# Kernel optimization log

Hardware: AMD Instinct MI355X
Metric: run time of the kernel (lower is better)

The kernel has to match this reference:

```python
import jax, jax.numpy as jnp
import numpy as np

# 27 kernel taps x 3 offset components (dz, dy, dx), matching the module's offset0 list.
OFFSET0 = np.array([
    1, 1, 1, 1, 1, 0, 1, 1, -1, 1, 0, 1, 1, 0, 0, 1, 0, -1, 1, -1, 1, 1, -1, 0, 1, -1, -1,
    0, 1, 1, 0, 1, 0, 0, 1, -1, 0, 0, 1, 0, 0, 0, 0, 0, -1, 0, -1, 1, 0, -1, 0, 0, -1, -1,
    -1, 1, 1, -1, 1, 0, -1, 1, -1, -1, 0, 1, -1, 0, 0, -1, 0, -1, -1, -1, 1, -1, -1, 0, -1, -1, -1
], dtype=np.float64).reshape(27, 3)

BN_EPS = 1e-5


def upsample_nearest2(x):
    # nn.Upsample(scale_factor=2), default mode='nearest', on [B,C,Z,Y,X]
    x = jnp.repeat(x, 2, axis=2)
    x = jnp.repeat(x, 2, axis=3)
    return jnp.repeat(x, 2, axis=4)


def deform_conv3d_static(x, W, b, alpha):
    """3D deformable conv, kernel 3, pad 1, stride 1, with spatially-constant
    per-tap offsets alpha*OFFSET0. Zero padding outside; trilinear sampling.
    Since offsets are static, each tap samples at a fixed fractional shift,
    implemented as a static trilinear combination of slices of the padded input.
    x: [B,C,Z,Y,X], W: [O,C,3,3,3], b: [O].
    """
    B, C, Z, Y, X = x.shape
    # pad 2: 1 for the 3x3x3 kernel + 1 for fractional offsets (|alpha*d| <= 0.7)
    xp = jnp.pad(x, ((0, 0), (0, 0), (2, 2), (2, 2), (2, 2)))
    out = None
    t = 0
    for kz in range(3):
        for ky in range(3):
            for kx in range(3):
                dz, dy, dx = (alpha * OFFSET0[t]).tolist()
                s = (kz - 1 + dz, ky - 1 + dy, kx - 1 + dx)  # shift rel. to output voxel
                f = [int(np.floor(v)) for v in s]
                w = [v - fl for v, fl in zip(s, f)]
                vol = None
                for cz in (0, 1):
                    for cy in (0, 1):
                        for cx in (0, 1):
                            wt = ((w[0] if cz else 1.0 - w[0]) *
                                  (w[1] if cy else 1.0 - w[1]) *
                                  (w[2] if cx else 1.0 - w[2]))
                            if wt == 0.0:
                                continue
                            z0 = 2 + f[0] + cz
                            y0 = 2 + f[1] + cy
                            x0 = 2 + f[2] + cx
                            sl = xp[:, :, z0:z0 + Z, y0:y0 + Y, x0:x0 + X]
                            sl = jnp.float32(wt) * sl
                            vol = sl if vol is None else vol + sl
                contrib = jnp.einsum('oc,bczyx->bozyx', W[:, :, kz, ky, kx], vol)
                out = contrib if out is None else out + contrib
                t += 1
    return out + b[None, :, None, None, None]


def batchnorm(x, g, bt, m, v):
    # eval-mode BatchNorm3d over channel axis 1
    inv = g * jax.lax.rsqrt(v + BN_EPS)
    return x * inv[None, :, None, None, None] + (bt - m * inv)[None, :, None, None, None]


def setup_inputs() -> dict:
    key = jax.random.key(0)
    ks = jax.random.split(key, 13)
    ch_in, ch_out = 64, 32
    x = jax.random.normal(ks[0], (1, ch_in, 32, 32, 32), jnp.float32)
    w_def = jax.random.normal(ks[1], (ch_out, ch_in, 3, 3, 3), jnp.float32) * 0.05
    b_def = jax.random.normal(ks[2], (ch_out,), jnp.float32) * 0.05
    bn1_g = 1.0 + 0.1 * jax.random.normal(ks[3], (ch_out,), jnp.float32)
    bn1_b = 0.1 * jax.random.normal(ks[4], (ch_out,), jnp.float32)
    bn1_m = 0.1 * jax.random.normal(ks[5], (ch_out,), jnp.float32)
    bn1_v = jax.random.uniform(ks[6], (ch_out,), jnp.float32, 0.5, 1.5)
    w_comb = jax.random.normal(ks[7], (ch_out, 3 * ch_out), jnp.float32) * 0.1
    b_comb = 0.05 * jax.random.normal(ks[8], (ch_out,), jnp.float32)
    bn2_g = 1.0 + 0.1 * jax.random.normal(ks[9], (ch_out,), jnp.float32)
    bn2_b = 0.1 * jax.random.normal(ks[10], (ch_out,), jnp.float32)
    bn2_m = 0.1 * jax.random.normal(ks[11], (ch_out,), jnp.float32)
    bn2_v = jax.random.uniform(ks[12], (ch_out,), jnp.float32, 0.5, 1.5)
    return {"x": x, "w_def": w_def, "b_def": b_def,
            "bn1_g": bn1_g, "bn1_b": bn1_b, "bn1_m": bn1_m, "bn1_v": bn1_v,
            "w_comb": w_comb, "b_comb": b_comb,
            "bn2_g": bn2_g, "bn2_b": bn2_b, "bn2_m": bn2_m, "bn2_v": bn2_v}


def reference(x, w_def, b_def, bn1_g, bn1_b, bn1_m, bn1_v,
              w_comb, b_comb, bn2_g, bn2_b, bn2_m, bn2_v):
    xu = upsample_nearest2(x)
    branches = []
    for alpha in (0.0, 0.4, 0.7):  # shared deform-conv weights, three static offset scales
        o = deform_conv3d_static(xu, w_def, b_def, alpha)
        o = jax.nn.relu(batchnorm(o, bn1_g, bn1_b, bn1_m, bn1_v))
        branches.append(o)
    cat = jnp.concatenate(branches, axis=1)  # [B, 3*ch_out, Z,Y,X]
    y = jnp.einsum('oc,bczyx->bozyx', w_comb, cat) + b_comb[None, :, None, None, None]
    y = batchnorm(y, bn2_g, bn2_b, bn2_m, bn2_v)
    return jax.nn.relu(y)
```

## Files before the change

kernel.cpp:

```cpp
#include <hip/hip_runtime.h>


typedef __bf16 bf16x8 __attribute__((ext_vector_type(8)));
typedef float f32x16 __attribute__((ext_vector_type(16)));
typedef unsigned u32x2 __attribute__((ext_vector_type(2)));

__device__ inline unsigned short f2bf(float f) {
  unsigned int u = __float_as_uint(f);
  u += 0x7FFFu + ((u >> 16) & 1u);
  return (unsigned short)(u >> 16);
}

__device__ inline bf16x8 bc16(uint4 v) { return __builtin_bit_cast(bf16x8, v); }

__device__ inline unsigned cvtpk(float lo, float hi) {
  unsigned r;
  asm("v_cvt_pk_bf16_f32 %0, %1, %2" : "=v"(r) : "v"(lo), "v"(hi));
  return r;
}

__device__ inline void plswap(unsigned& a, unsigned& b) {
  u32x2 r = __builtin_amdgcn_permlane32_swap(a, b, false, false);
  a = r.x;
  b = r.y;
}

__device__ inline void gload16(const unsigned short* g, unsigned short* l) {
  __builtin_amdgcn_global_load_lds(
      (const __attribute__((address_space(1))) unsigned int*)(const void*)g,
      (__attribute__((address_space(3))) unsigned int*)(void*)l, 16, 0, 0);
}

__device__ inline float ucoef(int abit, int k, int jbit, float alpha) {
  if (abit == 0) return (k == 0) ? (jbit ? alpha : 1.f - alpha) : (jbit ? 1.f : 0.f);
  return (k == 2) ? (jbit ? 1.f - alpha : alpha) : (jbit ? 0.f : 1.f);
}

__global__ void k_prep(const float* __restrict__ x, unsigned short* __restrict__ xT,
                       const float* __restrict__ w_def, const float* __restrict__ bn1_g,
                       const float* __restrict__ bn1_v, unsigned short* __restrict__ W_sw,
                       const float* __restrict__ w_comb, const float* __restrict__ b_comb,
                       const float* __restrict__ bn2_g, const float* __restrict__ bn2_b,
                       const float* __restrict__ bn2_m, const float* __restrict__ bn2_v,
                       const float* __restrict__ b_def, const float* __restrict__ bn1_b,
                       const float* __restrict__ bn1_m, unsigned short* __restrict__ W2_sw,
                       float* __restrict__ bias1, float* __restrict__ bias2) {
  __shared__ unsigned short t[64][65];
  int bid = blockIdx.x;
  if (bid < 512) {
    int s0 = bid * 64;
    int lane = threadIdx.x & 63;
    int grp = threadIdx.x >> 6;
#pragma unroll
    for (int c = grp; c < 64; c += 4)
      t[c][lane] = f2bf(x[c * 32768 + s0 + lane]);
    __syncthreads();
#pragma unroll
    for (int s = grp; s < 64; s += 4)
      xT[(size_t)(s0 + s) * 64 + lane] = t[lane][s];
  } else if (bid < 2048) {
    int e = (bid - 512) * 256 + threadIdx.x;
    int j = e & 7;
    int lane = (e >> 3) & 63;
    int idx = e >> 9;
    int nt = idx % 3;
    idx /= 3;
    int s = idx & 31;
    int p = idx >> 5;
    int o = lane & 31;
    int br = nt;
    int kk = 16 * s + ((lane >> 5) << 3) + j;
    int tap = kk >> 6, ch = kk & 63;
    int jz = (tap >> 2) & 1, jy = (tap >> 1) & 1, jx = tap & 1;
    int a = (p >> 2) & 1, b = (p >> 1) & 1, cp = p & 1;
    float alpha = (br == 0) ? 0.f : ((br == 1) ? 0.4f : 0.7f);
    const float* wb = w_def + (o * 64 + ch) * 27;
    float sum = 0.f;
    for (int kz = 0; kz < 3; ++kz) {
      float uz = ucoef(a, kz, jz, alpha);
      if (uz == 0.f) continue;
      for (int ky = 0; ky < 3; ++ky) {
        float uy = ucoef(b, ky, jy, alpha);
        if (uy == 0.f) continue;
        float uzy = uz * uy;
        for (int kx = 0; kx < 3; ++kx) {
          float ux = ucoef(cp, kx, jx, alpha);
          if (ux != 0.f) sum += wb[kz * 9 + ky * 3 + kx] * uzy * ux;
        }
      }
    }
    float s1 = bn1_g[o] * rsqrtf(bn1_v[o] + 1e-5f);
    W_sw[e] = f2bf(sum * s1);
  } else {
    int tid = threadIdx.x;
    for (int e = tid; e < 3072; e += 256) {
      int j = e & 7;
      int lane = (e >> 3) & 63;
      int s2 = e >> 9;
      int n = lane & 31;
      int k = 16 * s2 + ((lane >> 5) << 3) + j;
      float sc2 = bn2_g[n] * rsqrtf(bn2_v[n] + 1e-5f);
      W2_sw[e] = f2bf(w_comb[n * 96 + k] * sc2);
    }
    if (tid < 32) {
      float s1 = bn1_g[tid] * rsqrtf(bn1_v[tid] + 1e-5f);
      bias1[tid] = (b_def[tid] - bn1_m[tid]) * s1 + bn1_b[tid];
      float s2 = bn2_g[tid] * rsqrtf(bn2_v[tid] + 1e-5f);
      bias2[tid] = (b_comb[tid] - bn2_m[tid]) * s2 + bn2_b[tid];
    }
  }
}

__launch_bounds__(512, 2)
__global__ void k_main(const unsigned short* __restrict__ xT,
                       const unsigned short* __restrict__ W_sw,
                       const unsigned short* __restrict__ W2_sw,
                       const float* __restrict__ bias1f,
                       const float* __restrict__ bias2f,
                       float* __restrict__ out) {
  __shared__ unsigned short xt[51840];
  __shared__ unsigned short wring[2][12288];
  __shared__ float blds[64];
  int tid = threadIdx.x;
  int lane = tid & 63;
  int wv = tid >> 6;
  int bid = blockIdx.x;
  int bph = bid & 1, a = (bid >> 1) & 1;
  int tb = bid >> 2;
  int tx = tb & 3, ty = (tb >> 2) & 3, tz = tb >> 4;
  int i0 = tz * 8, j0 = ty * 8, k0 = tx * 8;

  for (int t2 = tid; t2 < 6480; t2 += 512) {
    int cblk = t2 & 7;
    int r = t2 >> 3;
    int xrel = r % 10;
    int zy = r / 10;
    int yrel = zy % 9;
    int zrel = zy / 9;
    int gz = i0 + a - 1 + zrel, gy = j0 + bph - 1 + yrel, gx = k0 - 1 + xrel;
    uint4 v = make_uint4(0u, 0u, 0u, 0u);
    if ((unsigned)gz < 32u && (unsigned)gy < 32u && (unsigned)gx < 32u)
      v = *(const uint4*)(xT + ((((gz * 32 + gy) * 32 + gx) << 6) + (cblk << 3)));
    *(uint4*)(xt + ((r << 6) + (((cblk + r) << 3) & 63))) = v;
  }
  if (tid < 32) {
    blds[tid] = bias1f[tid];
    blds[32 + tid] = bias2f[tid];
  }

  bf16x8 b2f[6];
  const uint4* w2q = (const uint4*)W2_sw;
#pragma unroll
  for (int s2 = 0; s2 < 6; ++s2) b2f[s2] = bc16(w2q[s2 * 64 + lane]);
  __syncthreads();

  int h = lane >> 5, h8 = h << 3;
  int m = lane & 31;
  int ax = m & 7, ay = (m >> 3) & 1, az = m >> 4;
  int zs = wv >> 2, ys = wv & 3;
  int dz0 = 4 * zs + az;
  int dy = 2 * ys + ay;
  int p0 = (a << 2) | (bph << 1);

  auto stage = [&](int cc) {
    int pn = p0 | (cc >> 2);
    const unsigned short* g =
        W_sw + (size_t)pn * 49152 + (cc & 3) * 12288 + wv * 1536 + lane * 8;
    unsigned short* l = &wring[cc & 1][wv * 1536];
    gload16(g, l);
    gload16(g + 512, l + 512);
    gload16(g + 1024, l + 1024);
  };

  stage(0);

  f32x16 osv0, osv1;
  f32x16 acc[2][3];
#pragma unroll
  for (int mt = 0; mt < 2; ++mt)
#pragma unroll
    for (int nt = 0; nt < 3; ++nt) acc[mt][nt] = (f32x16)0.f;

  int qr = (wv & 3) * 2;

  for (int cc = 0; cc < 8; ++cc) {
    asm volatile("s_waitcnt vmcnt(0)" ::: "memory");
    __builtin_amdgcn_s_barrier();
    __builtin_amdgcn_sched_barrier(0);
    if (cc < 7) stage(cc + 1);
    __builtin_amdgcn_sched_barrier(0);
    int cp = cc >> 2;
    int tb2 = (cc & 3) * 2;
    const unsigned short* wfb = &wring[cc & 1][lane * 8];
#pragma unroll
    for (int i = 0; i < 8; ++i) {
      int q2 = (i + qr) & 7;
      int tl = q2 >> 2, q = q2 & 3;
      int t8 = tb2 + tl;
      int jz = (t8 >> 2) & 1, jy = (t8 >> 1) & 1, jx = t8 & 1;
      int row0 = ((dz0 + jz) * 9 + (dy + jy)) * 10 + (ax + cp + jx);
      int row1 = row0 + 180;
      int c0 = (q << 4) + h8;
      int e0 = (row0 << 6) + ((c0 + (row0 << 3)) & 63);
      int e1 = (row1 << 6) + ((c0 + (row1 << 3)) & 63);
      bf16x8 a0 = bc16(*(const uint4*)(xt + e0));
      bf16x8 a1 = bc16(*(const uint4*)(xt + e1));
      const unsigned short* wf = wfb + tl * 6144 + q * 1536;
      bf16x8 bb0 = bc16(*(const uint4*)(wf));
      bf16x8 bb1 = bc16(*(const uint4*)(wf + 512));
      bf16x8 bb2 = bc16(*(const uint4*)(wf + 1024));
      __builtin_amdgcn_s_setprio(1);
      acc[0][0] = __builtin_amdgcn_mfma_f32_32x32x16_bf16(bb0, a0, acc[0][0], 0, 0, 0);
      acc[1][0] = __builtin_amdgcn_mfma_f32_32x32x16_bf16(bb0, a1, acc[1][0], 0, 0, 0);
      acc[0][1] = __builtin_amdgcn_mfma_f32_32x32x16_bf16(bb1, a0, acc[0][1], 0, 0, 0);
      acc[1][1] = __builtin_amdgcn_mfma_f32_32x32x16_bf16(bb1, a1, acc[1][1], 0, 0, 0);
      acc[0][2] = __builtin_amdgcn_mfma_f32_32x32x16_bf16(bb2, a0, acc[0][2], 0, 0, 0);
      acc[1][2] = __builtin_amdgcn_mfma_f32_32x32x16_bf16(bb2, a1, acc[1][2], 0, 0, 0);
      __builtin_amdgcn_s_setprio(0);
    }

    if (cc == 3) {
#pragma unroll
      for (int mt = 0; mt < 2; ++mt) {
        uint4 fr[6];
#pragma unroll
        for (int nt = 0; nt < 3; ++nt) {
          unsigned ww[8];
#pragma unroll
          for (int qc = 0; qc < 8; ++qc) {
            int q = qc >> 1, c2 = qc & 1;
            int r0 = 4 * q + 2 * c2;
            int row = (r0 & 3) + ((r0 >> 2) << 3) + (h << 2);
            float lo = fmaxf(acc[mt][nt][r0] + blds[row], 0.f);
            float hi = fmaxf(acc[mt][nt][r0 + 1] + blds[row + 1], 0.f);
            ww[2 * q + c2] = cvtpk(lo, hi);
          }
          plswap(ww[0], ww[2]);
          plswap(ww[1], ww[3]);
          plswap(ww[4], ww[6]);
          plswap(ww[5], ww[7]);
          fr[2 * nt] = make_uint4(ww[0], ww[1], ww[2], ww[3]);
          fr[2 * nt + 1] = make_uint4(ww[4], ww[5], ww[6], ww[7]);
        }
        f32x16 acc2 = (f32x16)0.f;
#pragma unroll
        for (int s2 = 0; s2 < 6; ++s2)
          acc2 = __builtin_amdgcn_mfma_f32_32x32x16_bf16(b2f[s2], bc16(fr[s2]), acc2, 0, 0, 0);
        f32x16 ov;
#pragma unroll
        for (int r = 0; r < 16; ++r) {
          int row = (r & 3) + ((r >> 2) << 3) + (h << 2);
          ov[r] = fmaxf(acc2[r] + blds[32 + row], 0.f);
        }
        if (mt == 0) osv0 = ov; else osv1 = ov;
#pragma unroll
        for (int nt = 0; nt < 3; ++nt) acc[mt][nt] = (f32x16)0.f;
      }
    }
  }

#pragma unroll
  for (int mt = 0; mt < 2; ++mt) {
    uint4 fr[6];
#pragma unroll
    for (int nt = 0; nt < 3; ++nt) {
      unsigned ww[8];
#pragma unroll
      for (int qc = 0; qc < 8; ++qc) {
        int q = qc >> 1, c2 = qc & 1;
        int r0 = 4 * q + 2 * c2;
        int row = (r0 & 3) + ((r0 >> 2) << 3) + (h << 2);
        float lo = fmaxf(acc[mt][nt][r0] + blds[row], 0.f);
        float hi = fmaxf(acc[mt][nt][r0 + 1] + blds[row + 1], 0.f);
        ww[2 * q + c2] = cvtpk(lo, hi);
      }
      plswap(ww[0], ww[2]);
      plswap(ww[1], ww[3]);
      plswap(ww[4], ww[6]);
      plswap(ww[5], ww[7]);
      fr[2 * nt] = make_uint4(ww[0], ww[1], ww[2], ww[3]);
      fr[2 * nt + 1] = make_uint4(ww[4], ww[5], ww[6], ww[7]);
    }
    f32x16 acc2 = (f32x16)0.f;
#pragma unroll
    for (int s2 = 0; s2 < 6; ++s2)
      acc2 = __builtin_amdgcn_mfma_f32_32x32x16_bf16(b2f[s2], bc16(fr[s2]), acc2, 0, 0, 0);
    f32x16 prev = (mt == 0) ? osv0 : osv1;
    int Z = 2 * (i0 + 4 * zs + 2 * mt + az) + a;
    int Y = 2 * (j0 + dy) + bph;
    float2* o2 = (float2*)out;
#pragma unroll
    for (int r = 0; r < 16; ++r) {
      int ch = (r & 3) + ((r >> 2) << 3) + (h << 2);
      float v1 = fmaxf(acc2[r] + blds[32 + ch], 0.f);
      o2[((size_t)ch << 17) + ((size_t)Z << 11) + (Y << 5) + (k0 + ax)] =
          make_float2(prev[r], v1);
    }
  }
}

extern "C" void kernel_launch(void* const* d_in, const int* in_sizes, int n_in,
                              void* d_out, int out_size, void* d_ws, size_t ws_size,
                              hipStream_t stream) {
  (void)in_sizes; (void)n_in; (void)out_size; (void)ws_size;
  const float* x      = (const float*)d_in[0];
  const float* w_def  = (const float*)d_in[1];
  const float* b_def  = (const float*)d_in[2];
  const float* bn1_g  = (const float*)d_in[3];
  const float* bn1_b  = (const float*)d_in[4];
  const float* bn1_m  = (const float*)d_in[5];
  const float* bn1_v  = (const float*)d_in[6];
  const float* w_comb = (const float*)d_in[7];
  const float* b_comb = (const float*)d_in[8];
  const float* bn2_g  = (const float*)d_in[9];
  const float* bn2_b  = (const float*)d_in[10];
  const float* bn2_m  = (const float*)d_in[11];
  const float* bn2_v  = (const float*)d_in[12];

  char* ws = (char*)d_ws;
  unsigned short* xT   = (unsigned short*)(ws);
  unsigned short* W_sw = (unsigned short*)(ws + 4194304);
  unsigned short* W2sw = (unsigned short*)(ws + 4980736);
  float* bias1 = (float*)(ws + 4986880);
  float* bias2 = (float*)(ws + 4987008);
  float* out = (float*)d_out;

  hipLaunchKernelGGL(k_prep, dim3(2049), dim3(256), 0, stream,
                     x, xT, w_def, bn1_g, bn1_v, W_sw,
                     w_comb, b_comb, bn2_g, bn2_b, bn2_m, bn2_v,
                     b_def, bn1_b, bn1_m, W2sw, bias1, bias2);
  hipLaunchKernelGGL(k_main, dim3(256), dim3(512), 0, stream,
                     xT, W_sw, W2sw, bias1, bias2, out);
}
```

Measured before the change: 52.91 us.

## Read input activations directly from global memory instead of an LDS halo tile

The LDS staging of the input halo tile is removed. The main kernel now loads MFMA A-fragments straight from a channel-quartered bf16 layout in global memory, with a zeroed pad region standing in for out-of-bounds voxels. Blocks shrink to 256 threads and the grid doubles to 512, with a reordered block-to-tile mapping. The second-stage weights are reloaded from global memory on demand rather than held in registers. This frees LDS and registers for occupancy and drops the staging loop, at the cost of more global and L2 traffic with less reuse of the halo across taps.

Result: no change. 53.74 us (+1.6%).

```diff
diff --git a/kernel.cpp b/kernel.cpp
--- a/kernel.cpp
+++ b/kernel.cpp
@@ -36,7 +36,10 @@
   return (k == 2) ? (jbit ? 1.f - alpha : alpha) : (jbit ? 0.f : 1.f);
 }
 
-__global__ void k_prep(const float* __restrict__ x, unsigned short* __restrict__ xT,
+#define XREG_USH 524352
+#define XZERO_B 1048576u
+
+__global__ void k_prep(const float* __restrict__ x, unsigned short* __restrict__ xT2,
                        const float* __restrict__ w_def, const float* __restrict__ bn1_g,
                        const float* __restrict__ bn1_v, unsigned short* __restrict__ W_sw,
                        const float* __restrict__ w_comb, const float* __restrict__ b_comb,
@@ -55,9 +58,10 @@
     for (int c = grp; c < 64; c += 4)
       t[c][lane] = f2bf(x[c * 32768 + s0 + lane]);
     __syncthreads();
+    int q = lane >> 4, e = lane & 15;
 #pragma unroll
     for (int s = grp; s < 64; s += 4)
-      xT[(size_t)(s0 + s) * 64 + lane] = t[lane][s];
+      xT2[q * XREG_USH + (size_t)(s0 + s) * 16 + e] = t[lane][s];
   } else if (bid < 2048) {
     int e = (bid - 512) * 256 + threadIdx.x;
     int j = e & 7;
@@ -102,6 +106,10 @@
       float sc2 = bn2_g[n] * rsqrtf(bn2_v[n] + 1e-5f);
       W2_sw[e] = f2bf(w_comb[n * 96 + k] * sc2);
     }
+    {
+      int q = tid >> 6, e2 = tid & 63;
+      xT2[q * XREG_USH + 524288 + e2] = 0;
+    }
     if (tid < 32) {
       float s1 = bn1_g[tid] * rsqrtf(bn1_v[tid] + 1e-5f);
       bias1[tid] = (b_def[tid] - bn1_m[tid]) * s1 + bn1_b[tid];
@@ -111,67 +119,51 @@
   }
 }
 
-__launch_bounds__(512, 2)
-__global__ void k_main(const unsigned short* __restrict__ xT,
+__launch_bounds__(256, 2)
+__global__ void k_main(const unsigned short* __restrict__ xT2,
                        const unsigned short* __restrict__ W_sw,
                        const unsigned short* __restrict__ W2_sw,
                        const float* __restrict__ bias1f,
                        const float* __restrict__ bias2f,
                        float* __restrict__ out) {
-  __shared__ unsigned short xt[51840];
   __shared__ unsigned short wring[2][12288];
   __shared__ float blds[64];
   int tid = threadIdx.x;
   int lane = tid & 63;
   int wv = tid >> 6;
   int bid = blockIdx.x;
-  int bph = bid & 1, a = (bid >> 1) & 1;
-  int tb = bid >> 2;
+  int tb = (bid & 7) | ((bid >> 5) << 3);
+  int ph = (bid >> 3) & 3;
+  int bph = ph & 1, a = ph >> 1;
   int tx = tb & 3, ty = (tb >> 2) & 3, tz = tb >> 4;
-  int i0 = tz * 8, j0 = ty * 8, k0 = tx * 8;
-
-  for (int t2 = tid; t2 < 6480; t2 += 512) {
-    int cblk = t2 & 7;
-    int r = t2 >> 3;
-    int xrel = r % 10;
-    int zy = r / 10;
-    int yrel = zy % 9;
-    int zrel = zy / 9;
-    int gz = i0 + a - 1 + zrel, gy = j0 + bph - 1 + yrel, gx = k0 - 1 + xrel;
-    uint4 v = make_uint4(0u, 0u, 0u, 0u);
-    if ((unsigned)gz < 32u && (unsigned)gy < 32u && (unsigned)gx < 32u)
-      v = *(const uint4*)(xT + ((((gz * 32 + gy) * 32 + gx) << 6) + (cblk << 3)));
-    *(uint4*)(xt + ((r << 6) + (((cblk + r) << 3) & 63))) = v;
-  }
+  int i0 = tz * 4, j0 = ty * 8, k0 = tx * 8;
+
   if (tid < 32) {
     blds[tid] = bias1f[tid];
     blds[32 + tid] = bias2f[tid];
   }
 
-  bf16x8 b2f[6];
-  const uint4* w2q = (const uint4*)W2_sw;
-#pragma unroll
-  for (int s2 = 0; s2 < 6; ++s2) b2f[s2] = bc16(w2q[s2 * 64 + lane]);
-  __syncthreads();
-
-  int h = lane >> 5, h8 = h << 3;
+  int h = lane >> 5;
   int m = lane & 31;
   int ax = m & 7, ay = (m >> 3) & 1, az = m >> 4;
-  int zs = wv >> 2, ys = wv & 3;
-  int dz0 = 4 * zs + az;
-  int dy = 2 * ys + ay;
   int p0 = (a << 2) | (bph << 1);
+  unsigned hb = (unsigned)(h << 4);
+
+  const char* xq0 = (const char*)xT2;
+  const char* xq1 = xq0 + 1048704;
+  const char* xq2 = xq0 + 2097408;
+  const char* xq3 = xq0 + 3146112;
 
   auto stage = [&](int cc) {
     int pn = p0 | (cc >> 2);
     const unsigned short* g =
-        W_sw + (size_t)pn * 49152 + (cc & 3) * 12288 + wv * 1536 + lane * 8;
-    unsigned short* l = &wring[cc & 1][wv * 1536];
-    gload16(g, l);
-    gload16(g + 512, l + 512);
-    gload16(g + 1024, l + 1024);
+        W_sw + pn * 49152 + (cc & 3) * 12288 + wv * 3072 + lane * 8;
+    unsigned short* l = &wring[cc & 1][wv * 3072];
+#pragma unroll
+    for (int k = 0; k < 6; ++k) gload16(g + k * 512, l + k * 512);
   };
 
+  __syncthreads();
   stage(0);
 
   f32x16 osv0, osv1;
@@ -180,8 +172,6 @@
   for (int mt = 0; mt < 2; ++mt)
 #pragma unroll
     for (int nt = 0; nt < 3; ++nt) acc[mt][nt] = (f32x16)0.f;
-
-  int qr = (wv & 3) * 2;
 
   for (int cc = 0; cc < 8; ++cc) {
     asm volatile("s_waitcnt vmcnt(0)" ::: "memory");
@@ -189,37 +179,52 @@
     __builtin_amdgcn_sched_barrier(0);
     if (cc < 7) stage(cc + 1);
     __builtin_amdgcn_sched_barrier(0);
-    int cp = cc >> 2;
-    int tb2 = (cc & 3) * 2;
+
+    int cp = cc >> 2, jy = cc & 1, jz = (cc >> 1) & 1;
+    int gz0i = i0 + a - 1 + az + jz;
+    int gz1i = gz0i + 2;
+    int gyi = j0 + bph - 1 + 2 * wv + ay + jy;
+    int gx0i = k0 - 1 + ax + cp;
+    int gx1i = gx0i + 1;
+    bool oky = (unsigned)gyi < 32u;
+    bool okz0 = (unsigned)gz0i < 32u, okz1 = (unsigned)gz1i < 32u;
+    bool okx0 = (unsigned)gx0i < 32u, okx1 = (unsigned)gx1i < 32u;
+    unsigned s00 = (unsigned)(((gz0i * 32 + gyi) * 32 + gx0i) * 32) + hb;
+    unsigned s01 = (unsigned)(((gz1i * 32 + gyi) * 32 + gx0i) * 32) + hb;
+    unsigned s10 = (unsigned)(((gz0i * 32 + gyi) * 32 + gx1i) * 32) + hb;
+    unsigned s11 = (unsigned)(((gz1i * 32 + gyi) * 32 + gx1i) * 32) + hb;
+    unsigned v00 = (oky && okz0 && okx0) ? s00 : XZERO_B;
+    unsigned v01 = (oky && okz1 && okx0) ? s01 : XZERO_B;
+    unsigned v10 = (oky && okz0 && okx1) ? s10 : XZERO_B;
+    unsigned v11 = (oky && okz1 && okx1) ? s11 : XZERO_B;
+
     const unsigned short* wfb = &wring[cc & 1][lane * 8];
 #pragma unroll
-    for (int i = 0; i < 8; ++i) {
-      int q2 = (i + qr) & 7;
-      int tl = q2 >> 2, q = q2 & 3;
-      int t8 = tb2 + tl;
-      int jz = (t8 >> 2) & 1, jy = (t8 >> 1) & 1, jx = t8 & 1;
-      int row0 = ((dz0 + jz) * 9 + (dy + jy)) * 10 + (ax + cp + jx);
-      int row1 = row0 + 180;
-      int c0 = (q << 4) + h8;
-      int e0 = (row0 << 6) + ((c0 + (row0 << 3)) & 63);
-      int e1 = (row1 << 6) + ((c0 + (row1 << 3)) & 63);
-      bf16x8 a0 = bc16(*(const uint4*)(xt + e0));
-      bf16x8 a1 = bc16(*(const uint4*)(xt + e1));
-      const unsigned short* wf = wfb + tl * 6144 + q * 1536;
-      bf16x8 bb0 = bc16(*(const uint4*)(wf));
-      bf16x8 bb1 = bc16(*(const uint4*)(wf + 512));
-      bf16x8 bb2 = bc16(*(const uint4*)(wf + 1024));
-      __builtin_amdgcn_s_setprio(1);
-      acc[0][0] = __builtin_amdgcn_mfma_f32_32x32x16_bf16(bb0, a0, acc[0][0], 0, 0, 0);
-      acc[1][0] = __builtin_amdgcn_mfma_f32_32x32x16_bf16(bb0, a1, acc[1][0], 0, 0, 0);
-      acc[0][1] = __builtin_amdgcn_mfma_f32_32x32x16_bf16(bb1, a0, acc[0][1], 0, 0, 0);
-      acc[1][1] = __builtin_amdgcn_mfma_f32_32x32x16_bf16(bb1, a1, acc[1][1], 0, 0, 0);
-      acc[0][2] = __builtin_amdgcn_mfma_f32_32x32x16_bf16(bb2, a0, acc[0][2], 0, 0, 0);
-      acc[1][2] = __builtin_amdgcn_mfma_f32_32x32x16_bf16(bb2, a1, acc[1][2], 0, 0, 0);
-      __builtin_amdgcn_s_setprio(0);
+    for (int tl = 0; tl < 2; ++tl) {
+      unsigned va0 = tl ? v10 : v00;
+      unsigned va1 = tl ? v11 : v01;
+#pragma unroll
+      for (int q = 0; q < 4; ++q) {
+        const char* xb = (q == 0) ? xq0 : (q == 1) ? xq1 : (q == 2) ? xq2 : xq3;
+        bf16x8 a0 = bc16(*(const uint4*)(xb + va0));
+        bf16x8 a1 = bc16(*(const uint4*)(xb + va1));
+        const unsigned short* wf = wfb + tl * 6144 + q * 1536;
+        bf16x8 bb0 = bc16(*(const uint4*)(wf));
+        bf16x8 bb1 = bc16(*(const uint4*)(wf + 512));
+        bf16x8 bb2 = bc16(*(const uint4*)(wf + 1024));
+        __builtin_amdgcn_s_setprio(1);
+        acc[0][0] = __builtin_amdgcn_mfma_f32_32x32x16_bf16(bb0, a0, acc[0][0], 0, 0, 0);
+        acc[1][0] = __builtin_amdgcn_mfma_f32_32x32x16_bf16(bb0, a1, acc[1][0], 0, 0, 0);
+        acc[0][1] = __builtin_amdgcn_mfma_f32_32x32x16_bf16(bb1, a0, acc[0][1], 0, 0, 0);
+        acc[1][1] = __builtin_amdgcn_mfma_f32_32x32x16_bf16(bb1, a1, acc[1][1], 0, 0, 0);
+        acc[0][2] = __builtin_amdgcn_mfma_f32_32x32x16_bf16(bb2, a0, acc[0][2], 0, 0, 0);
+        acc[1][2] = __builtin_amdgcn_mfma_f32_32x32x16_bf16(bb2, a1, acc[1][2], 0, 0, 0);
+        __builtin_amdgcn_s_setprio(0);
+      }
     }
 
     if (cc == 3) {
+      const uint4* w2q = (const uint4*)W2_sw;
 #pragma unroll
       for (int mt = 0; mt < 2; ++mt) {
         uint4 fr[6];
@@ -245,7 +250,8 @@
         f32x16 acc2 = (f32x16)0.f;
 #pragma unroll
         for (int s2 = 0; s2 < 6; ++s2)
-          acc2 = __builtin_amdgcn_mfma_f32_32x32x16_bf16(b2f[s2], bc16(fr[s2]), acc2, 0, 0, 0);
+          acc2 = __builtin_amdgcn_mfma_f32_32x32x16_bf16(bc16(w2q[s2 * 64 + lane]),
+                                                         bc16(fr[s2]), acc2, 0, 0, 0);
         f32x16 ov;
 #pragma unroll
         for (int r = 0; r < 16; ++r) {
@@ -259,42 +265,46 @@
     }
   }
 
-#pragma unroll
-  for (int mt = 0; mt < 2; ++mt) {
-    uint4 fr[6];
-#pragma unroll
-    for (int nt = 0; nt < 3; ++nt) {
-      unsigned ww[8];
-#pragma unroll
-      for (int qc = 0; qc < 8; ++qc) {
-        int q = qc >> 1, c2 = qc & 1;
-        int r0 = 4 * q + 2 * c2;
-        int row = (r0 & 3) + ((r0 >> 2) << 3) + (h << 2);
-        float lo = fmaxf(acc[mt][nt][r0] + blds[row], 0.f);
-        float hi = fmaxf(acc[mt][nt][r0 + 1] + blds[row + 1], 0.f);
-        ww[2 * q + c2] = cvtpk(lo, hi);
-      }
-      plswap(ww[0], ww[2]);
-      plswap(ww[1], ww[3]);
-      plswap(ww[4], ww[6]);
-      plswap(ww[5], ww[7]);
-      fr[2 * nt] = make_uint4(ww[0], ww[1], ww[2], ww[3]);
-      fr[2 * nt + 1] = make_uint4(ww[4], ww[5], ww[6], ww[7]);
-    }
-    f32x16 acc2 = (f32x16)0.f;
-#pragma unroll
-    for (int s2 = 0; s2 < 6; ++s2)
-      acc2 = __builtin_amdgcn_mfma_f32_32x32x16_bf16(b2f[s2], bc16(fr[s2]), acc2, 0, 0, 0);
-    f32x16 prev = (mt == 0) ? osv0 : osv1;
-    int Z = 2 * (i0 + 4 * zs + 2 * mt + az) + a;
-    int Y = 2 * (j0 + dy) + bph;
-    float2* o2 = (float2*)out;
-#pragma unroll
-    for (int r = 0; r < 16; ++r) {
-      int ch = (r & 3) + ((r >> 2) << 3) + (h << 2);
-      float v1 = fmaxf(acc2[r] + blds[32 + ch], 0.f);
-      o2[((size_t)ch << 17) + ((size_t)Z << 11) + (Y << 5) + (k0 + ax)] =
-          make_float2(prev[r], v1);
+  {
+    const uint4* w2q = (const uint4*)W2_sw;
+#pragma unroll
+    for (int mt = 0; mt < 2; ++mt) {
+      uint4 fr[6];
+#pragma unroll
+      for (int nt = 0; nt < 3; ++nt) {
+        unsigned ww[8];
+#pragma unroll
+        for (int qc = 0; qc < 8; ++qc) {
+          int q = qc >> 1, c2 = qc & 1;
+          int r0 = 4 * q + 2 * c2;
+          int row = (r0 & 3) + ((r0 >> 2) << 3) + (h << 2);
+          float lo = fmaxf(acc[mt][nt][r0] + blds[row], 0.f);
+          float hi = fmaxf(acc[mt][nt][r0 + 1] + blds[row + 1], 0.f);
+          ww[2 * q + c2] = cvtpk(lo, hi);
+        }
+        plswap(ww[0], ww[2]);
+        plswap(ww[1], ww[3]);
+        plswap(ww[4], ww[6]);
+        plswap(ww[5], ww[7]);
+        fr[2 * nt] = make_uint4(ww[0], ww[1], ww[2], ww[3]);
+        fr[2 * nt + 1] = make_uint4(ww[4], ww[5], ww[6], ww[7]);
+      }
+      f32x16 acc2 = (f32x16)0.f;
+#pragma unroll
+      for (int s2 = 0; s2 < 6; ++s2)
+        acc2 = __builtin_amdgcn_mfma_f32_32x32x16_bf16(bc16(w2q[s2 * 64 + lane]),
+                                                       bc16(fr[s2]), acc2, 0, 0, 0);
+      f32x16 prev = (mt == 0) ? osv0 : osv1;
+      int Z = 2 * (i0 + 2 * mt + az) + a;
+      int Y = 2 * (j0 + 2 * wv + ay) + bph;
+      float2* o2 = (float2*)out;
+#pragma unroll
+      for (int r = 0; r < 16; ++r) {
+        int ch = (r & 3) + ((r >> 2) << 3) + (h << 2);
+        float v1 = fmaxf(acc2[r] + blds[32 + ch], 0.f);
+        o2[((size_t)ch << 17) + ((size_t)Z << 11) + (Y << 5) + (k0 + ax)] =
+            make_float2(prev[r], v1);
+      }
     }
   }
 }
@@ -318,17 +328,17 @@
   const float* bn2_v  = (const float*)d_in[12];
 
   char* ws = (char*)d_ws;
-  unsigned short* xT   = (unsigned short*)(ws);
-  unsigned short* W_sw = (unsigned short*)(ws + 4194304);
-  unsigned short* W2sw = (unsigned short*)(ws + 4980736);
-  float* bias1 = (float*)(ws + 4986880);
-  float* bias2 = (float*)(ws + 4987008);
+  unsigned short* xT2  = (unsigned short*)(ws);
+  unsigned short* W_sw = (unsigned short*)(ws + 4194816);
+  unsigned short* W2sw = (unsigned short*)(ws + 4981248);
+  float* bias1 = (float*)(ws + 4987392);
+  float* bias2 = (float*)(ws + 4987520);
   float* out = (float*)d_out;
 
   hipLaunchKernelGGL(k_prep, dim3(2049), dim3(256), 0, stream,
-                     x, xT, w_def, bn1_g, bn1_v, W_sw,
+                     x, xT2, w_def, bn1_g, bn1_v, W_sw,
                      w_comb, b_comb, bn2_g, bn2_b, bn2_m, bn2_v,
                      b_def, bn1_b, bn1_m, W2sw, bias1, bias2);
-  hipLaunchKernelGGL(k_main, dim3(256), dim3(512), 0, stream,
-                     xT, W_sw, W2sw, bias1, bias2, out);
-}
+  hipLaunchKernelGGL(k_main, dim3(512), dim3(256), 0, stream,
+                     xT2, W_sw, W2sw, bias1, bias2, out);
+}
```

## Use triple-buffered weight ring with finer chunks and prefetch depth two

Applied to the files above, without the earlier changes.

Replaces the double-buffered weight staging (8 chunks of two taps each) with a triple-buffered ring of 16 single-tap chunks, prefetching two chunks ahead and waiting with vmcnt(2) instead of draining all loads each iteration. Only six of the eight waves issue the global-to-LDS loads. The per-wave rotation of the tap/quarter order (qr) is dropped. The aim is to hide weight-load latency behind MFMA work, at the cost of twice as many barriers and less compute between them, plus possible LDS bank conflicts now that all waves read in the same order.

Measured after the change: 52.72 us, median of 2. About the same (-0.4%).

```diff
diff --git a/kernel.cpp b/kernel.cpp
--- a/kernel.cpp
+++ b/kernel.cpp
@@ -119,7 +119,7 @@
                        const float* __restrict__ bias2f,
                        float* __restrict__ out) {
   __shared__ unsigned short xt[51840];
-  __shared__ unsigned short wring[2][12288];
+  __shared__ unsigned short wring[3][6144];
   __shared__ float blds[64];
   int tid = threadIdx.x;
   int lane = tid & 63;
@@ -162,17 +162,19 @@
   int dy = 2 * ys + ay;
   int p0 = (a << 2) | (bph << 1);
 
-  auto stage = [&](int cc) {
-    int pn = p0 | (cc >> 2);
-    const unsigned short* g =
-        W_sw + (size_t)pn * 49152 + (cc & 3) * 12288 + wv * 1536 + lane * 8;
-    unsigned short* l = &wring[cc & 1][wv * 1536];
-    gload16(g, l);
-    gload16(g + 512, l + 512);
-    gload16(g + 1024, l + 1024);
+  auto stage = [&](int c, int slot) {
+    if (wv < 6) {
+      int pn = p0 | (c >> 3);
+      const unsigned short* g =
+          W_sw + (size_t)pn * 49152 + (c & 7) * 6144 + wv * 1024 + lane * 8;
+      unsigned short* l = &wring[slot][wv * 1024];
+      gload16(g, l);
+      gload16(g + 512, l + 512);
+    }
   };
 
-  stage(0);
+  stage(0, 0);
+  stage(1, 1);
 
   f32x16 osv0, osv1;
   f32x16 acc[2][3];
@@ -181,31 +183,30 @@
 #pragma unroll
     for (int nt = 0; nt < 3; ++nt) acc[mt][nt] = (f32x16)0.f;
 
-  int qr = (wv & 3) * 2;
-
-  for (int cc = 0; cc < 8; ++cc) {
-    asm volatile("s_waitcnt vmcnt(0)" ::: "memory");
+  for (int c = 0; c < 16; ++c) {
+    if (c < 15) {
+      asm volatile("s_waitcnt vmcnt(2)" ::: "memory");
+    } else {
+      asm volatile("s_waitcnt vmcnt(0)" ::: "memory");
+    }
     __builtin_amdgcn_s_barrier();
     __builtin_amdgcn_sched_barrier(0);
-    if (cc < 7) stage(cc + 1);
+    if (c < 14) stage(c + 2, (c + 2) % 3);
     __builtin_amdgcn_sched_barrier(0);
-    int cp = cc >> 2;
-    int tb2 = (cc & 3) * 2;
-    const unsigned short* wfb = &wring[cc & 1][lane * 8];
-#pragma unroll
-    for (int i = 0; i < 8; ++i) {
-      int q2 = (i + qr) & 7;
-      int tl = q2 >> 2, q = q2 & 3;
-      int t8 = tb2 + tl;
-      int jz = (t8 >> 2) & 1, jy = (t8 >> 1) & 1, jx = t8 & 1;
-      int row0 = ((dz0 + jz) * 9 + (dy + jy)) * 10 + (ax + cp + jx);
-      int row1 = row0 + 180;
+
+    int cp = c >> 3, t8 = c & 7;
+    int jz = (t8 >> 2) & 1, jy = (t8 >> 1) & 1, jx = t8 & 1;
+    int row0 = ((dz0 + jz) * 9 + (dy + jy)) * 10 + (ax + cp + jx);
+    int row1 = row0 + 180;
+    const unsigned short* wfb = &wring[c % 3][lane * 8];
+#pragma unroll
+    for (int q = 0; q < 4; ++q) {
       int c0 = (q << 4) + h8;
       int e0 = (row0 << 6) + ((c0 + (row0 << 3)) & 63);
       int e1 = (row1 << 6) + ((c0 + (row1 << 3)) & 63);
       bf16x8 a0 = bc16(*(const uint4*)(xt + e0));
       bf16x8 a1 = bc16(*(const uint4*)(xt + e1));
-      const unsigned short* wf = wfb + tl * 6144 + q * 1536;
+      const unsigned short* wf = wfb + q * 1536;
       bf16x8 bb0 = bc16(*(const uint4*)(wf));
       bf16x8 bb1 = bc16(*(const uint4*)(wf + 512));
       bf16x8 bb2 = bc16(*(const uint4*)(wf + 1024));
@@ -219,7 +220,7 @@
       __builtin_amdgcn_s_setprio(0);
     }
 
-    if (cc == 3) {
+    if (c == 7) {
 #pragma unroll
       for (int mt = 0; mt < 2; ++mt) {
         uint4 fr[6];
```
